# Kernel optimization log

Hardware: AMD Instinct MI355X
Metric: run time of the kernel (lower is better)

The kernel has to match this reference:

```python
import jax, jax.numpy as jnp
import numpy as np

D_IN = 1024
D_OUT = 1024
NUM_HEADS = 16
HEAD_DIM = D_OUT // NUM_HEADS


def setup_inputs() -> dict:
    key = jax.random.key(0)
    ks = jax.random.split(key, 9)
    s = 0.02
    return {
        "x": jax.random.normal(ks[0], (2, 2048, D_IN), dtype=jnp.float32),
        "Wq": jax.random.normal(ks[1], (D_IN, D_OUT), dtype=jnp.float32) * s,
        "bq": jnp.zeros((D_OUT,), dtype=jnp.float32),
        "Wk": jax.random.normal(ks[2], (D_IN, D_OUT), dtype=jnp.float32) * s,
        "bk": jnp.zeros((D_OUT,), dtype=jnp.float32),
        "Wv": jax.random.normal(ks[3], (D_IN, D_OUT), dtype=jnp.float32) * s,
        "bv": jnp.zeros((D_OUT,), dtype=jnp.float32),
        "Wo": jax.random.normal(ks[4], (D_OUT, D_OUT), dtype=jnp.float32) * s,
        "bo": jnp.zeros((D_OUT,), dtype=jnp.float32),
    }


def reference(x, Wq, bq, Wk, bk, Wv, bv, Wo, bo):
    B, S, _ = x.shape
    H, Dh = NUM_HEADS, HEAD_DIM
    q = (x @ Wq + bq).reshape(B, S, H, Dh).transpose(0, 2, 1, 3)  # bhsd
    k = (x @ Wk + bk).reshape(B, S, H, Dh).transpose(0, 2, 1, 3)
    v = (x @ Wv + bv).reshape(B, S, H, Dh).transpose(0, 2, 1, 3)
    scores = jnp.einsum("bhqd,bhkd->bhqk", q, k) * (Dh ** -0.5)
    causal = jnp.tril(jnp.ones((S, S), dtype=bool))
    scores = jnp.where(causal, scores, jnp.float32(-jnp.inf))
    w = jax.nn.softmax(scores, axis=-1)
    ctx = jnp.einsum("bhqk,bhkd->bhqd", w, v)
    ctx = ctx.transpose(0, 2, 1, 3).reshape(B, S, H * Dh)
    return ctx @ Wo + bo
```

## Files before the change

kernel.cpp:

```cpp
#include <hip/hip_runtime.h>
#include <cmath>

#define D_IN 1024
#define D_OUT 1024
#define NUM_HEADS 16
#define HEAD_DIM 64
#define BATCH 2
#define SEQ 2048
#define GK 1024
#define KT 32

typedef __attribute__((ext_vector_type(8))) short short8;
typedef __attribute__((ext_vector_type(4))) short short4v;
typedef __attribute__((ext_vector_type(4))) float float4v;

__device__ __forceinline__ unsigned short f2bf(float f) {
  unsigned int u = __builtin_bit_cast(unsigned int, f);
  unsigned int r = (u + 0x7FFFu + ((u >> 16) & 1u)) >> 16;
  return (unsigned short)r;
}
__device__ __forceinline__ float bf2f(unsigned short h) {
  return __builtin_bit_cast(float, (unsigned int)h << 16);
}

__device__ __forceinline__ void async_copy16(void* lds, const void* g) {
  __builtin_amdgcn_global_load_lds(
      (const __attribute__((address_space(1))) unsigned int*)g,
      (__attribute__((address_space(3))) unsigned int*)lds, 16, 0, 0);
}

#define DPP_F(x, ctrl) __builtin_bit_cast(float,                         \
    __builtin_amdgcn_update_dpp(__builtin_bit_cast(int, (x)),            \
                                __builtin_bit_cast(int, (x)),            \
                                (ctrl), 0xF, 0xF, false))

__device__ __forceinline__ float red16_sum(float x) {
  x += DPP_F(x, 0xB1);
  x += DPP_F(x, 0x4E);
  x += DPP_F(x, 0x124);
  x += DPP_F(x, 0x128);
  return x;
}

__global__ __launch_bounds__(256) void prep(
    const float* __restrict__ x, const float* __restrict__ Wq,
    const float* __restrict__ Wk, const float* __restrict__ Wv,
    const float* __restrict__ Wo, unsigned short* __restrict__ xb,
    unsigned short* __restrict__ wqkv_t, unsigned short* __restrict__ wo_t) {
  const int z = blockIdx.z;
  if (z == 4) {
    const int bid = blockIdx.y * 32 + blockIdx.x;
    const size_t i0 = ((size_t)bid * 256 + threadIdx.x) * 16;
#pragma unroll
    for (int half = 0; half < 2; ++half) {
      const size_t o = i0 + half * 8;
      float4 a = *(const float4*)(x + o);
      float4 b = *(const float4*)(x + o + 4);
      union { unsigned short u[8]; short8 v; } t;
      t.u[0] = f2bf(a.x); t.u[1] = f2bf(a.y); t.u[2] = f2bf(a.z); t.u[3] = f2bf(a.w);
      t.u[4] = f2bf(b.x); t.u[5] = f2bf(b.y); t.u[6] = f2bf(b.z); t.u[7] = f2bf(b.w);
      *(short8*)(xb + o) = t.v;
    }
    return;
  }
  const float* W = (z == 0) ? Wq : (z == 1) ? Wk : (z == 2) ? Wv : Wo;
  unsigned short* out = (z < 3) ? (wqkv_t + (size_t)z * 1024 * 1024) : wo_t;

  __shared__ float T[32][33];
  const int r = threadIdx.x >> 3;
  const int c4 = (threadIdx.x & 7) << 2;
  const int k0 = blockIdx.x * 32, n0 = blockIdx.y * 32;

  float4 v = *(const float4*)(W + (size_t)(k0 + r) * 1024 + n0 + c4);
  T[r][c4 + 0] = v.x; T[r][c4 + 1] = v.y; T[r][c4 + 2] = v.z; T[r][c4 + 3] = v.w;
  __syncthreads();

  union { unsigned short u[4]; short4v v4; } o;
#pragma unroll
  for (int i = 0; i < 4; ++i) o.u[i] = f2bf(T[c4 + i][r]);
  *(short4v*)(out + (size_t)(n0 + r) * 1024 + k0 + c4) = o.v4;
}

__device__ __forceinline__ void gemm_core(
    const unsigned short* __restrict__ A, const unsigned short* __restrict__ Bt,
    unsigned short* As, unsigned short* Bs, int bm, int bn, float4v acc[4][4]) {
  const int tid = threadIdx.x;
  const int wave = tid >> 6, lane = tid & 63;
  const int quad = lane >> 4, l16 = lane & 15;
  const int wr = wave >> 1, wc = wave & 1;
  const int sw = l16 & 7;

  int srow[4], sgc[4];
#pragma unroll
  for (int t = 0; t < 4; ++t) {
    const int c = (wave * 4 + t) * 64 + lane;
    srow[t] = c >> 3;
    sgc[t] = ((c & 7) ^ (srow[t] & 7)) * 8;
  }

  for (int k0 = 0; k0 < GK; k0 += 64) {
    __syncthreads();
#pragma unroll
    for (int t = 0; t < 4; ++t) {
      const int c = (wave * 4 + t) * 64 + lane;
      async_copy16(As + (size_t)c * 8, A + (size_t)(bm + srow[t]) * GK + k0 + sgc[t]);
    }
#pragma unroll
    for (int t = 0; t < 4; ++t) {
      const int c = (wave * 4 + t) * 64 + lane;
      async_copy16(Bs + (size_t)c * 8, Bt + (size_t)(bn + srow[t]) * GK + k0 + sgc[t]);
    }
    __syncthreads();

#pragma unroll
    for (int h = 0; h < 2; ++h) {
      short8 af[4], bf[4];
#pragma unroll
      for (int i = 0; i < 4; ++i) {
        const int row = wr * 64 + i * 16 + l16;
        af[i] = *(const short8*)&As[((size_t)row * 8 + ((h * 4 + quad) ^ sw)) * 8];
      }
#pragma unroll
      for (int j = 0; j < 4; ++j) {
        const int row = wc * 64 + j * 16 + l16;
        bf[j] = *(const short8*)&Bs[((size_t)row * 8 + ((h * 4 + quad) ^ sw)) * 8];
      }
#pragma unroll
      for (int i = 0; i < 4; ++i)
#pragma unroll
        for (int j = 0; j < 4; ++j)
          acc[i][j] = __builtin_amdgcn_mfma_f32_16x16x32_bf16(af[i], bf[j], acc[i][j], 0, 0, 0);
    }
  }
}

__global__ __launch_bounds__(256) void gemm_qkv(
    const unsigned short* __restrict__ A, const unsigned short* __restrict__ Bt,
    const float* __restrict__ bq, const float* __restrict__ bk,
    const float* __restrict__ bv,
    unsigned short* __restrict__ qbuf, unsigned short* __restrict__ kblk,
    unsigned short* __restrict__ vblk) {
  __shared__ unsigned short As[128 * 64];
  __shared__ unsigned short Bs[128 * 64];
  const int wave = threadIdx.x >> 6, lane = threadIdx.x & 63;
  const int quad = lane >> 4, l16 = lane & 15;
  const int wr = wave >> 1, wc = wave & 1;
  const int bm = blockIdx.x * 128, bn = blockIdx.y * 128;

  float4v acc[4][4] = {};
  gemm_core(A, Bt, As, Bs, bm, bn, acc);

#pragma unroll
  for (int j = 0; j < 4; ++j) {
    const int n = bn + wc * 64 + j * 16 + l16;
    const int seg = n >> 10, nn = n & 1023;
    const int h = nn >> 6, d = nn & 63;
    const float bsv = (seg == 0) ? bq[nn] : (seg == 1) ? bk[nn] : bv[nn];
    const float scale = (seg == 0) ? 0.18033688011112043f : 1.0f;
#pragma unroll
    for (int i = 0; i < 4; ++i) {
#pragma unroll
      for (int r = 0; r < 4; ++r) {
        const int m = bm + wr * 64 + i * 16 + quad * 4 + r;
        const int b = m >> 11, s = m & 2047;
        const int bh = b * NUM_HEADS + h;
        const unsigned short hv = f2bf((acc[i][j][r] + bsv) * scale);
        if (seg == 0) {
          qbuf[((size_t)bh * SEQ + s) * HEAD_DIM + d] = hv;
        } else if (seg == 1) {
          kblk[((size_t)bh * 64 + (s >> 5)) * 2048 +
               (size_t)(((((s >> 4) & 1) * 2 + (d >> 5)) * 64 +
                         ((d >> 3) & 3) * 16 + (s & 15)) * 8 + (d & 7))] = hv;
        } else {
          vblk[((size_t)bh * 64 + (s >> 5)) * 2048 +
               (size_t)(((d >> 4) * 64 + ((s >> 3) & 3) * 16 + (d & 15)) * 8 +
                        (s & 7))] = hv;
        }
      }
    }
  }
}

__global__ __launch_bounds__(256) void gemm_out(
    const unsigned short* __restrict__ A, const unsigned short* __restrict__ Bt,
    const float* __restrict__ bo, float* __restrict__ out) {
  __shared__ unsigned short As[128 * 64];
  __shared__ unsigned short Bs[128 * 64];
  const int wave = threadIdx.x >> 6, lane = threadIdx.x & 63;
  const int quad = lane >> 4, l16 = lane & 15;
  const int wr = wave >> 1, wc = wave & 1;
  const int bm = blockIdx.x * 128, bn = blockIdx.y * 128;

  float4v acc[4][4] = {};
  gemm_core(A, Bt, As, Bs, bm, bn, acc);

#pragma unroll
  for (int j = 0; j < 4; ++j) {
    const int n = bn + wc * 64 + j * 16 + l16;
    const float bsv = bo[n];
#pragma unroll
    for (int i = 0; i < 4; ++i) {
#pragma unroll
      for (int r = 0; r < 4; ++r) {
        const int m = bm + wr * 64 + i * 16 + quad * 4 + r;
        out[(size_t)m * D_OUT + n] = acc[i][j][r] + bsv;
      }
    }
  }
}

#define OBS 72

__global__ __launch_bounds__(256) void attn_kernel(
    const unsigned short* __restrict__ qf, const unsigned short* __restrict__ kblk,
    const unsigned short* __restrict__ vblk, unsigned short* __restrict__ ctx) {
  __shared__ unsigned short PL[4 * 32 * 40];
  __shared__ unsigned short OB[4 * 32 * OBS];
  __shared__ float LL[4 * 32];

  const int id = blockIdx.x;
  const int bh = id & 31;
  const int qblk = 63 - (id >> 5);
  const int qw0 = qblk * 32;
  const int tid = threadIdx.x;
  const int w = tid >> 6;
  const int lane = tid & 63;
  const int quad = lane >> 4;
  const int l16 = lane & 15;

  const int nt = qblk + 1;
  const int qch = (nt + 3) >> 2;
  const int t0 = w * qch;
  const int t1 = min(nt, t0 + qch);

  const size_t bh_base = (size_t)bh * SEQ * HEAD_DIM;
  const unsigned short* kb = kblk + bh_base;
  const unsigned short* vb = vblk + bh_base;

  short8 aq[2][2];
#pragma unroll
  for (int qt = 0; qt < 2; ++qt) {
    const unsigned short* qrow =
        qf + bh_base + (size_t)(qw0 + qt * 16 + l16) * HEAD_DIM + quad * 8;
    aq[qt][0] = *(const short8*)qrow;
    aq[qt][1] = *(const short8*)(qrow + 32);
  }

  float4v O[2][4] = {};
  float l_part[2][4] = {};
  unsigned short* PLw = PL + w * (32 * 40);

  if (t0 < t1) {
    short8 kA[4], vA[4], kB[4], vB[4];

    auto load = [&](int kt, short8 kd[4], short8 vd[4]) {
      const size_t base = (size_t)kt * 2048 + lane * 8;
#pragma unroll
      for (int f = 0; f < 4; ++f) kd[f] = *(const short8*)(kb + base + f * 512);
#pragma unroll
      for (int f = 0; f < 4; ++f) vd[f] = *(const short8*)(vb + base + f * 512);
    };

    auto step = [&](int kt, const short8 kd[4], const short8 vd[4], bool masked) {
      const int k0 = kt * KT;
      float4v cs[2][2];
#pragma unroll
      for (int qt = 0; qt < 2; ++qt)
#pragma unroll
        for (int g = 0; g < 2; ++g) {
          float4v c = {0.f, 0.f, 0.f, 0.f};
          c = __builtin_amdgcn_mfma_f32_16x16x32_bf16(aq[qt][0], kd[2 * g], c, 0, 0, 0);
          c = __builtin_amdgcn_mfma_f32_16x16x32_bf16(aq[qt][1], kd[2 * g + 1], c, 0, 0, 0);
          cs[qt][g] = c;
        }

#pragma unroll
      for (int qt = 0; qt < 2; ++qt)
#pragma unroll
        for (int g = 0; g < 2; ++g)
#pragma unroll
          for (int r = 0; r < 4; ++r) {
            float s = cs[qt][g][r];
            if (masked) {
              const int key = k0 + g * 16 + l16;
              const int qg = qw0 + qt * 16 + quad * 4 + r;
              s = (key <= qg) ? s : -1e30f;
            }
            const float p = __builtin_exp2f(s);
            l_part[qt][r] += p;
            const unsigned int pu = __builtin_bit_cast(unsigned int, p);
            PLw[(qt * 16 + quad * 4 + r) * 40 + (g * 2 + (l16 >> 3)) * 8 + (l16 & 7)] =
                (unsigned short)(pu >> 16);
          }

#pragma unroll
      for (int qt = 0; qt < 2; ++qt) {
        const short8 pA = *(const short8*)&PLw[(qt * 16 + l16) * 40 + quad * 8];
#pragma unroll
        for (int jj = 0; jj < 4; ++jj)
          O[qt][jj] = __builtin_amdgcn_mfma_f32_16x16x32_bf16(pA, vd[jj], O[qt][jj], 0, 0, 0);
      }
    };

    load(t0, kA, vA);
    int kt = t0;
    while (true) {
      const bool lastA = (kt == t1 - 1);
      if (!lastA) load(kt + 1, kB, vB);
      step(kt, kA, vA, kt == nt - 1);
      if (lastA) break;
      ++kt;
      const bool lastB = (kt == t1 - 1);
      if (!lastB) load(kt + 1, kA, vA);
      step(kt, kB, vB, kt == nt - 1);
      if (lastB) break;
      ++kt;
    }
  }

#pragma unroll
  for (int qt = 0; qt < 2; ++qt)
#pragma unroll
    for (int r = 0; r < 4; ++r) {
      const float lsum = red16_sum(l_part[qt][r]);
      const int row = qt * 16 + quad * 4 + r;
      if (l16 == 0) LL[w * 32 + row] = lsum;
#pragma unroll
      for (int jj = 0; jj < 4; ++jj)
        OB[(w * 32 + row) * OBS + jj * 16 + l16] = f2bf(O[qt][jj][r]);
    }

  __syncthreads();

  const int row = w * 8 + (lane >> 3);
  const int col0 = (lane & 7) * 8;
  float acc[8] = {};
#pragma unroll
  for (int u = 0; u < 4; ++u) {
    const short8 t = *(const short8*)&OB[(u * 32 + row) * OBS + col0];
#pragma unroll
    for (int i = 0; i < 8; ++i) acc[i] += bf2f((unsigned short)t[i]);
  }
  const float inv = 1.0f / (LL[row] + LL[32 + row] + LL[64 + row] + LL[96 + row]);
  union { unsigned short u[8]; short8 v; } o;
#pragma unroll
  for (int i = 0; i < 8; ++i) o.u[i] = f2bf(acc[i] * inv);
  const int b = bh >> 4, h = bh & 15;
  const int qg = qw0 + row;
  *(short8*)(ctx + ((size_t)b * SEQ + qg) * D_OUT + h * HEAD_DIM + col0) = o.v;
}

extern "C" void kernel_launch(void* const* d_in, const int* in_sizes, int n_in,
                              void* d_out, int out_size, void* d_ws, size_t ws_size,
                              hipStream_t stream) {
  const float* x  = (const float*)d_in[0];
  const float* Wq = (const float*)d_in[1];
  const float* bq = (const float*)d_in[2];
  const float* Wk = (const float*)d_in[3];
  const float* bk = (const float*)d_in[4];
  const float* Wv = (const float*)d_in[5];
  const float* bv = (const float*)d_in[6];
  const float* Wo = (const float*)d_in[7];
  const float* bo = (const float*)d_in[8];
  float* out = (float*)d_out;

  const int M = BATCH * SEQ;
  unsigned short* xb     = (unsigned short*)d_ws;
  unsigned short* wqkv_t = xb + (size_t)M * D_IN;
  unsigned short* wo_t   = wqkv_t + (size_t)3 * D_OUT * D_IN;
  unsigned short* qb     = wo_t + (size_t)D_OUT * D_OUT;
  unsigned short* kblk   = qb + (size_t)M * D_OUT;
  unsigned short* vblk   = kblk + (size_t)M * D_OUT;
  unsigned short* cb     = vblk + (size_t)M * D_OUT;

  prep<<<dim3(32, 32, 5), 256, 0, stream>>>(x, Wq, Wk, Wv, Wo, xb, wqkv_t, wo_t);
  gemm_qkv<<<dim3(M / 128, 3 * D_OUT / 128), 256, 0, stream>>>(
      xb, wqkv_t, bq, bk, bv, qb, kblk, vblk);
  attn_kernel<<<dim3(32 * 64), 256, 0, stream>>>(qb, kblk, vblk, cb);
  gemm_out<<<dim3(M / 128, D_OUT / 128), 256, 0, stream>>>(cb, wo_t, bo, out);
}
```

Measured before the change: 208.4 us.

## Switch attention to 32x32x16 MFMA with register-resident P via permlane swap

Reworks the attention inner loop to use 32x32x16 bf16 MFMAs. Scores are computed transposed (K as the A operand, Q as B) so each lane holds one query column. P is converted to bf16 with v_cvt_pk_bf16_f32 and rearranged across lane halves with permlane32_swap, which removes the LDS round trip for P and the per-row DPP reductions. The K/V block layouts written by the QKV GEMM epilogue change to match the new fragment ordering. The cost is inline asm and a gfx950-specific permlane intrinsic, plus more VGPRs held in 16-wide accumulators.

```diff
diff --git a/kernel.cpp b/kernel.cpp
--- a/kernel.cpp
+++ b/kernel.cpp
@@ -13,6 +13,8 @@
 typedef __attribute__((ext_vector_type(8))) short short8;
 typedef __attribute__((ext_vector_type(4))) short short4v;
 typedef __attribute__((ext_vector_type(4))) float float4v;
+typedef __attribute__((ext_vector_type(16))) float f32x16;
+typedef __attribute__((ext_vector_type(2))) int int2v;
 
 __device__ __forceinline__ unsigned short f2bf(float f) {
   unsigned int u = __builtin_bit_cast(unsigned int, f);
@@ -23,23 +25,16 @@
   return __builtin_bit_cast(float, (unsigned int)h << 16);
 }
 
+__device__ __forceinline__ unsigned int cvtpk(float lo, float hi) {
+  unsigned int r;
+  asm("v_cvt_pk_bf16_f32 %0, %1, %2" : "=v"(r) : "v"(lo), "v"(hi));
+  return r;
+}
+
 __device__ __forceinline__ void async_copy16(void* lds, const void* g) {
   __builtin_amdgcn_global_load_lds(
       (const __attribute__((address_space(1))) unsigned int*)g,
       (__attribute__((address_space(3))) unsigned int*)lds, 16, 0, 0);
-}
-
-#define DPP_F(x, ctrl) __builtin_bit_cast(float,                         \
-    __builtin_amdgcn_update_dpp(__builtin_bit_cast(int, (x)),            \
-                                __builtin_bit_cast(int, (x)),            \
-                                (ctrl), 0xF, 0xF, false))
-
-__device__ __forceinline__ float red16_sum(float x) {
-  x += DPP_F(x, 0xB1);
-  x += DPP_F(x, 0x4E);
-  x += DPP_F(x, 0x124);
-  x += DPP_F(x, 0x128);
-  return x;
 }
 
 __global__ __launch_bounds__(256) void prep(
@@ -169,12 +164,11 @@
           qbuf[((size_t)bh * SEQ + s) * HEAD_DIM + d] = hv;
         } else if (seg == 1) {
           kblk[((size_t)bh * 64 + (s >> 5)) * 2048 +
-               (size_t)(((((s >> 4) & 1) * 2 + (d >> 5)) * 64 +
-                         ((d >> 3) & 3) * 16 + (s & 15)) * 8 + (d & 7))] = hv;
+               (size_t)((d >> 4) * 512 + (((d >> 3) & 1) * 32 + (s & 31)) * 8 + (d & 7))] = hv;
         } else {
           vblk[((size_t)bh * 64 + (s >> 5)) * 2048 +
-               (size_t)(((d >> 4) * 64 + ((s >> 3) & 3) * 16 + (d & 15)) * 8 +
-                        (s & 7))] = hv;
+               (size_t)(((((s >> 4) & 1) * 2 + (d >> 5)) * 512) +
+                        (((s >> 3) & 1) * 32 + (d & 31)) * 8 + (s & 7))] = hv;
         }
       }
     }
@@ -214,7 +208,6 @@
 __global__ __launch_bounds__(256) void attn_kernel(
     const unsigned short* __restrict__ qf, const unsigned short* __restrict__ kblk,
     const unsigned short* __restrict__ vblk, unsigned short* __restrict__ ctx) {
-  __shared__ unsigned short PL[4 * 32 * 40];
   __shared__ unsigned short OB[4 * 32 * OBS];
   __shared__ float LL[4 * 32];
 
@@ -225,8 +218,8 @@
   const int tid = threadIdx.x;
   const int w = tid >> 6;
   const int lane = tid & 63;
-  const int quad = lane >> 4;
-  const int l16 = lane & 15;
+  const int l32 = lane & 31;
+  const int hi = lane >> 5;
 
   const int nt = qblk + 1;
   const int qch = (nt + 3) >> 2;
@@ -234,27 +227,25 @@
   const int t1 = min(nt, t0 + qch);
 
   const size_t bh_base = (size_t)bh * SEQ * HEAD_DIM;
-  const unsigned short* kb = kblk + bh_base;
-  const unsigned short* vb = vblk + bh_base;
-
-  short8 aq[2][2];
-#pragma unroll
-  for (int qt = 0; qt < 2; ++qt) {
+  const unsigned short* kb = kblk + bh_base + (size_t)lane * 8;
+  const unsigned short* vb = vblk + bh_base + (size_t)lane * 8;
+
+  short8 qfr[4];
+  {
     const unsigned short* qrow =
-        qf + bh_base + (size_t)(qw0 + qt * 16 + l16) * HEAD_DIM + quad * 8;
-    aq[qt][0] = *(const short8*)qrow;
-    aq[qt][1] = *(const short8*)(qrow + 32);
-  }
-
-  float4v O[2][4] = {};
-  float l_part[2][4] = {};
-  unsigned short* PLw = PL + w * (32 * 40);
+        qf + bh_base + (size_t)(qw0 + l32) * HEAD_DIM + hi * 8;
+#pragma unroll
+    for (int f = 0; f < 4; ++f) qfr[f] = *(const short8*)(qrow + f * 16);
+  }
+
+  f32x16 O0 = {}, O1 = {};
+  float l_part = 0.f;
 
   if (t0 < t1) {
     short8 kA[4], vA[4], kB[4], vB[4];
 
     auto load = [&](int kt, short8 kd[4], short8 vd[4]) {
-      const size_t base = (size_t)kt * 2048 + lane * 8;
+      const size_t base = (size_t)kt * 2048;
 #pragma unroll
       for (int f = 0; f < 4; ++f) kd[f] = *(const short8*)(kb + base + f * 512);
 #pragma unroll
@@ -262,44 +253,51 @@
     };
 
     auto step = [&](int kt, const short8 kd[4], const short8 vd[4], bool masked) {
-      const int k0 = kt * KT;
-      float4v cs[2][2];
-#pragma unroll
-      for (int qt = 0; qt < 2; ++qt)
-#pragma unroll
-        for (int g = 0; g < 2; ++g) {
-          float4v c = {0.f, 0.f, 0.f, 0.f};
-          c = __builtin_amdgcn_mfma_f32_16x16x32_bf16(aq[qt][0], kd[2 * g], c, 0, 0, 0);
-          c = __builtin_amdgcn_mfma_f32_16x16x32_bf16(aq[qt][1], kd[2 * g + 1], c, 0, 0, 0);
-          cs[qt][g] = c;
+      (void)kt;
+      f32x16 s = {};
+#pragma unroll
+      for (int f = 0; f < 4; ++f)
+        s = __builtin_amdgcn_mfma_f32_32x32x16_bf16(kd[f], qfr[f], s, 0, 0, 0);
+
+      float p[16];
+#pragma unroll
+      for (int g = 0; g < 4; ++g)
+#pragma unroll
+        for (int r = 0; r < 4; ++r) {
+          float sv = s[g * 4 + r];
+          if (masked) {
+            const int krow = r + 8 * g + 4 * hi;
+            sv = (krow <= l32) ? sv : -1e30f;
+          }
+          const float pv = __builtin_exp2f(sv);
+          p[g * 4 + r] = pv;
+          l_part += pv;
         }
 
-#pragma unroll
-      for (int qt = 0; qt < 2; ++qt)
-#pragma unroll
-        for (int g = 0; g < 2; ++g)
-#pragma unroll
-          for (int r = 0; r < 4; ++r) {
-            float s = cs[qt][g][r];
-            if (masked) {
-              const int key = k0 + g * 16 + l16;
-              const int qg = qw0 + qt * 16 + quad * 4 + r;
-              s = (key <= qg) ? s : -1e30f;
-            }
-            const float p = __builtin_exp2f(s);
-            l_part[qt][r] += p;
-            const unsigned int pu = __builtin_bit_cast(unsigned int, p);
-            PLw[(qt * 16 + quad * 4 + r) * 40 + (g * 2 + (l16 >> 3)) * 8 + (l16 & 7)] =
-                (unsigned short)(pu >> 16);
-          }
-
-#pragma unroll
-      for (int qt = 0; qt < 2; ++qt) {
-        const short8 pA = *(const short8*)&PLw[(qt * 16 + l16) * 40 + quad * 8];
-#pragma unroll
-        for (int jj = 0; jj < 4; ++jj)
-          O[qt][jj] = __builtin_amdgcn_mfma_f32_16x16x32_bf16(pA, vd[jj], O[qt][jj], 0, 0, 0);
-      }
+      unsigned int c[8];
+#pragma unroll
+      for (int g = 0; g < 4; ++g) {
+        c[g * 2 + 0] = cvtpk(p[g * 4 + 0], p[g * 4 + 1]);
+        c[g * 2 + 1] = cvtpk(p[g * 4 + 2], p[g * 4 + 3]);
+      }
+      {
+        int2v r0 = __builtin_amdgcn_permlane32_swap((int)c[0], (int)c[2], false, false);
+        c[0] = (unsigned int)r0.x; c[2] = (unsigned int)r0.y;
+        int2v r1 = __builtin_amdgcn_permlane32_swap((int)c[1], (int)c[3], false, false);
+        c[1] = (unsigned int)r1.x; c[3] = (unsigned int)r1.y;
+        int2v r2 = __builtin_amdgcn_permlane32_swap((int)c[4], (int)c[6], false, false);
+        c[4] = (unsigned int)r2.x; c[6] = (unsigned int)r2.y;
+        int2v r3 = __builtin_amdgcn_permlane32_swap((int)c[5], (int)c[7], false, false);
+        c[5] = (unsigned int)r3.x; c[7] = (unsigned int)r3.y;
+      }
+      union { unsigned int d[4]; short8 v; } pa0, pa1;
+      pa0.d[0] = c[0]; pa0.d[1] = c[1]; pa0.d[2] = c[2]; pa0.d[3] = c[3];
+      pa1.d[0] = c[4]; pa1.d[1] = c[5]; pa1.d[2] = c[6]; pa1.d[3] = c[7];
+
+      O0 = __builtin_amdgcn_mfma_f32_32x32x16_bf16(pa0.v, vd[0], O0, 0, 0, 0);
+      O1 = __builtin_amdgcn_mfma_f32_32x32x16_bf16(pa0.v, vd[1], O1, 0, 0, 0);
+      O0 = __builtin_amdgcn_mfma_f32_32x32x16_bf16(pa1.v, vd[2], O0, 0, 0, 0);
+      O1 = __builtin_amdgcn_mfma_f32_32x32x16_bf16(pa1.v, vd[3], O1, 0, 0, 0);
     };
 
     load(t0, kA, vA);
@@ -318,16 +316,16 @@
     }
   }
 
-#pragma unroll
-  for (int qt = 0; qt < 2; ++qt)
+  const float lsum = l_part + __shfl_xor(l_part, 32);
+  if (hi == 0) LL[w * 32 + l32] = lsum;
+#pragma unroll
+  for (int g = 0; g < 4; ++g)
 #pragma unroll
     for (int r = 0; r < 4; ++r) {
-      const float lsum = red16_sum(l_part[qt][r]);
-      const int row = qt * 16 + quad * 4 + r;
-      if (l16 == 0) LL[w * 32 + row] = lsum;
-#pragma unroll
-      for (int jj = 0; jj < 4; ++jj)
-        OB[(w * 32 + row) * OBS + jj * 16 + l16] = f2bf(O[qt][jj][r]);
+      const int reg = g * 4 + r;
+      const int row = r + 8 * g + 4 * hi;
+      OB[(w * 32 + row) * OBS + l32] = f2bf(O0[reg]);
+      OB[(w * 32 + row) * OBS + 32 + l32] = f2bf(O1[reg]);
     }
 
   __syncthreads();
```

Result: faster. 193.7 us (-7.1%).
